# Kernel optimization log

Hardware: AMD Instinct MI355X
Metric: run time of the kernel (lower is better)

The kernel has to match this reference:

```python
import jax, jax.numpy as jnp
import numpy as np

BLOCK = 32      # config.BLOCK_SIZE
PSF_WN = 64     # config.PSF_WINDOW_N (upsampled block size == PSF kernel size)
DX = 1e-06      # config.PIX_SIZE


def images_to_blocks(imgs, B):
    # Faithful to torch reshape/permute chain: block order is (nBW outer, nBH inner)
    N, H, W = imgs.shape
    nBH, nBW = H // B, W // B
    x = imgs.reshape(N, nBH, B, nBW, B)
    x = jnp.transpose(x, (0, 2, 4, 3, 1))        # [N,B,B,nBW,nBH]
    x = x.reshape(N, B, B, nBW * nBH)
    return jnp.transpose(x, (0, 3, 1, 2))        # [N,P,B,B]


def upsample_nearest(blocks, U):
    # torch F.interpolate(mode='nearest'): src index = floor(dst * B / U)
    N, P, B, _ = blocks.shape
    idx = (jnp.arange(U) * B) // U
    return blocks[:, :, idx[:, None], idx[None, :]]  # [N,P,U,U]


def depthwise_full_conv(x, w):
    # per-region cross-correlation with padding K-1 ("full"), groups=P
    N, P, K, _ = x.shape
    return jax.lax.conv_general_dilated(
        x, w[:, None, :, :], window_strides=(1, 1),
        padding=[(K - 1, K - 1), (K - 1, K - 1)],
        dimension_numbers=('NCHW', 'OIHW', 'NCHW'),
        feature_group_count=P)                   # [N,P,2K-1,2K-1]


def splat_blocks_to_sensor(block_out, x_centers, y_centers, X_N, Y_N, dx):
    # Vectorized scatter-add replacing the per-region python loop; out-of-bounds dropped
    N, P, Hk, Wk = block_out.shape
    hk = Hk // 2
    cx, cy = X_N // 2, Y_N // 2
    ic = cx + jnp.round(x_centers / dx).astype(jnp.int32)   # [P]
    jc = cy + jnp.round(y_centers / dx).astype(jnp.int32)
    I = ic[:, None] - hk + jnp.arange(Hk)                   # [P,Hk]
    J = jc[:, None] - hk + jnp.arange(Wk)                   # [P,Wk]
    lin = I[:, :, None] * Y_N + J[:, None, :]               # [P,Hk,Wk]
    ok = ((I >= 0) & (I < X_N))[:, :, None] & ((J >= 0) & (J < Y_N))[:, None, :]
    lin = jnp.where(ok, lin, -1).reshape(-1)
    sensor = jnp.zeros((N, X_N * Y_N), block_out.dtype)
    sensor = sensor.at[:, lin].add(block_out.reshape(N, -1), mode='drop')
    return sensor.reshape(N, X_N, Y_N)


def setup_inputs() -> dict:
    key = jax.random.key(0)
    k1, k2 = jax.random.split(key)
    N, H, W = 8, 512, 512
    P = (H // BLOCK) * (W // BLOCK)   # 256
    X_N = Y_N = 1024
    imgs = jax.random.uniform(k1, (N, H, W), jnp.float32)
    psf_stack = jax.random.uniform(k2, (P, PSF_WN, PSF_WN), jnp.float32)
    psf_stack = psf_stack / jnp.sum(psf_stack, axis=(1, 2), keepdims=True)
    # 16x16 grid of physical region centers, 48-pixel pitch (integer pixels so round() is exact)
    grid = jnp.arange(P)
    rows = (grid % 16).astype(jnp.float32)
    cols = (grid // 16).astype(jnp.float32)
    x_centers = (rows - 7.0) * 48.0 * DX
    y_centers = (cols - 7.0) * 48.0 * DX
    Xg, Yg = jnp.meshgrid(jnp.arange(X_N, dtype=jnp.float32) * DX,
                          jnp.arange(Y_N, dtype=jnp.float32) * DX, indexing='ij')
    return {"imgs": imgs, "psf_stack": psf_stack, "X": Xg, "Y": Yg,
            "x_centers": x_centers, "y_centers": y_centers}


def reference(imgs, psf_stack, X, Y, x_centers, y_centers):
    blocks = images_to_blocks(imgs, BLOCK)               # [N,P,32,32]
    blocks_up = upsample_nearest(blocks, PSF_WN)         # [N,P,64,64]
    block_out = depthwise_full_conv(blocks_up, psf_stack)  # [N,P,127,127]
    X_N, Y_N = X.shape
    return splat_blocks_to_sensor(block_out, x_centers, y_centers, X_N, Y_N, DX)
```

## Files before the change

### kernel.cpp

```cpp
#include <hip/hip_runtime.h>

typedef _Float16 h8 __attribute__((ext_vector_type(8)));
typedef float    f4 __attribute__((ext_vector_type(4)));
typedef unsigned int u4 __attribute__((ext_vector_type(4)));

#define IMG_N 8
#define IMG_H 512
#define IMG_W 512
#define P_CNT 256
#define PSFN  64
#define SENS  1024

#define TILE_HALVES 16256
#define TILES_BYTES ((size_t)IMG_N * P_CNT * TILE_HALVES * 2)

#define KW     90
#define KFRAG_PER_P (4 * 33 * KW)

#define BT_COLS   97
#define BT_HALVES (BT_COLS * 40)

__global__ __launch_bounds__(256) void svconv_prep(
    const float* __restrict__ psf, u4* __restrict__ kfrag)
{
    __shared__ float ps[PSFN * PSFN];
    __shared__ float Kc[4 * 33 * 33];
    const int p = blockIdx.x, tid = threadIdx.x;

    const float4* pp = (const float4*)(psf + (size_t)p * PSFN * PSFN);
    float4* pd = (float4*)ps;
    for (int i = tid; i < PSFN * PSFN / 4; i += 256) pd[i] = pp[i];
    __syncthreads();

    for (int idx = tid; idx < 4 * 33 * 33; idx += 256) {
        const int g = idx % 33, e = (idx / 33) % 33, cls = idx / 1089;
        const int pi = cls >> 1, pj = cls & 1;
        const int E = pi ? 32 : 33;
        float sv = 0.f;
        if (e < E) {
            const int a = 2 * e - 1 + pi, b = 2 * g - 1 + pj;
            #pragma unroll
            for (int du = 0; du < 2; ++du) {
                const int x = a + du;
                if ((unsigned)x < 64u) {
                    #pragma unroll
                    for (int dv = 0; dv < 2; ++dv) {
                        const int y = b + dv;
                        if ((unsigned)y < 64u) sv += ps[x * 64 + y];
                    }
                }
            }
        }
        Kc[idx] = sv;
    }
    __syncthreads();

    u4* kout = kfrag + (size_t)p * KFRAG_PER_P;
    for (int idx = tid; idx < KFRAG_PER_P; idx += 256) {
        const int w = idx % KW;
        const int g = (idx / KW) % 33;
        const int cls = idx / (KW * 33);
        h8 hv;
        #pragma unroll
        for (int j = 0; j < 8; ++j) {
            const int e = w + j - 32;
            const float v = ((unsigned)e < 33u) ? Kc[cls * 1089 + e * 33 + g] : 0.f;
            hv[j] = (_Float16)v;
        }
        kout[idx] = __builtin_bit_cast(u4, hv);
    }
}

__global__ __launch_bounds__(256, 4) void svconv_main(
    const float* __restrict__ imgs, const u4* __restrict__ kfrag,
    _Float16* __restrict__ tiles)
{
    __shared__ __align__(16) _Float16 BT[BT_HALVES];

    const int bid = blockIdx.x;
    const int n = bid >> 8, p = bid & 255;
    const int bh = p & 15, bw = p >> 4;
    const int tid = threadIdx.x;
    const int wv = tid >> 6, lane = tid & 63;
    const int m = lane & 15, q = lane >> 4;

    for (int i = tid; i < BT_HALVES; i += 256) BT[i] = (_Float16)0.f;
    __syncthreads();
    {
        const int r0 = tid >> 5, c = tid & 31;
        const float* src = imgs + ((size_t)n * IMG_H + bh * 32) * IMG_W + bw * 32;
        for (int r = r0; r < 32; r += 8)
            BT[(c + 32) * 40 + r] = (_Float16)src[r * IMG_W + c];
    }
    __syncthreads();

    const int cls = wv, pi = cls >> 1, pj = cls & 1;
    const int U0 = pi ? 31 : 32;
    const char* btc = (const char*)BT + pj * 80;

    int boff[4];
    #pragma unroll
    for (int vt = 0; vt < 4; ++vt) boff[vt] = (16 * vt + m) * 80 + q * 16;

    const char* ka[4];
    {
        const char* base = (const char*)(kfrag + (size_t)p * KFRAG_PER_P
                                         + cls * 33 * KW);
        #pragma unroll
        for (int ut = 0; ut < 4; ++ut) {
            const int t0 = 8 * q - m + (U0 - 16 * ut) + 32;
            ka[ut] = base + t0 * 16;
        }
    }

    f4 acc[4][4];
    #pragma unroll
    for (int ut = 0; ut < 4; ++ut)
        #pragma unroll
        for (int vt = 0; vt < 4; ++vt) acc[ut][vt] = (f4){0.f, 0.f, 0.f, 0.f};

    #pragma unroll 3
    for (int g = 0; g < 33; ++g) {
        h8 A[4];
        #pragma unroll
        for (int ut = 0; ut < 4; ++ut)
            A[ut] = __builtin_bit_cast(h8, *(const u4*)(ka[ut] + g * (KW * 16)));
        h8 B[4];
        #pragma unroll
        for (int vt = 0; vt < 4; ++vt)
            B[vt] = *(const h8*)(btc + boff[vt] + g * 80);
        #pragma unroll
        for (int ut = 0; ut < 4; ++ut)
            #pragma unroll
            for (int vt = 0; vt < 4; ++vt)
                acc[ut][vt] = __builtin_amdgcn_mfma_f32_16x16x32_f16(
                    A[ut], B[vt], acc[ut][vt], 0, 0, 0);
    }

    _Float16* tile = tiles + (size_t)(n * P_CNT + p) * TILE_HALVES;
    const int plane = pi ? (8192 + pj * 4032) : (pj * 4096);
    #pragma unroll
    for (int ut = 0; ut < 4; ++ut) {
        #pragma unroll
        for (int reg = 0; reg < 4; ++reg) {
            const int u = 16 * ut + 4 * q + reg;
            if (pi == 0 || u < 63) {
                _Float16* rp = tile + plane + u * 64 + m;
                #pragma unroll
                for (int vt = 0; vt < 4; ++vt)
                    rp[16 * vt] = (_Float16)acc[ut][vt][reg];
            }
        }
    }
}

__global__ __launch_bounds__(256) void svconv_gather(
    const _Float16* __restrict__ ws, float* __restrict__ out)
{
    const int b = blockIdx.x;
    const int n = b >> 10, x = b & 1023;
    int bhlo = (x + 288) / 48 - 10; if (bhlo < 0) bhlo = 0;
    int bhhi = (x < 113) ? -1 : ((x - 113) / 48);
    if (bhhi > 15) bhhi = 15;
    const _Float16* wsn = ws + (size_t)n * P_CNT * TILE_HALVES;
    float* outrow = out + ((size_t)n << 20) + (size_t)x * SENS;

    for (int yb = 0; yb < 4; ++yb) {
        const int y = yb * 256 + threadIdx.x;
        int bwlo = (y + 288) / 48 - 10; if (bwlo < 0) bwlo = 0;
        int bwhi = (y < 113) ? -1 : ((y - 113) / 48);
        if (bwhi > 15) bwhi = 15;
        float s = 0.0f;
        for (int bhh = bhlo; bhh <= bhhi; ++bhh) {
            const int ti = x - 113 - 48 * bhh;
            const int pi = ti & 1, uu = ti >> 1;
            for (int bww = bwlo; bww <= bwhi; ++bww) {
                const int tj = y - 113 - 48 * bww;
                const int pj = tj & 1, vv = tj >> 1;
                const int base = pi ? (8192 + pj * 4032) : (pj * 4096);
                s += (float)wsn[(size_t)(bww * 16 + bhh) * TILE_HALVES
                                + base + uu * 64 + vv];
            }
        }
        outrow[y] = s;
    }
}

extern "C" void kernel_launch(void* const* d_in, const int* in_sizes, int n_in,
                              void* d_out, int out_size, void* d_ws, size_t ws_size,
                              hipStream_t stream) {
    const float* imgs = (const float*)d_in[0];
    const float* psf  = (const float*)d_in[1];
    float* out = (float*)d_out;
    _Float16* tiles = (_Float16*)d_ws;
    u4* kfrag = (u4*)((char*)d_ws + TILES_BYTES);

    svconv_prep<<<dim3(P_CNT), dim3(256), 0, stream>>>(psf, kfrag);
    svconv_main<<<dim3(IMG_N * P_CNT), dim3(256), 0, stream>>>(imgs, kfrag, tiles);
    svconv_gather<<<dim3(IMG_N * SENS), dim3(256), 0, stream>>>(tiles, out);
}
```

Before: 228.3 us.

## Stage gather tile rows in LDS, double-buffer kernel fragments, split prep

The gather kernel now loads the up to 3x16 tile rows each output row needs into shared memory with 16-byte vector loads, then sums overlapping tiles from LDS. Out-of-range tiles are redirected to a zero slot instead of looping with variable bounds. This replaces scattered 2-byte global reads. The main MFMA loop is fully unrolled with double-buffered register prefetch of the A fragments to hide global load latency. The prep kernel is split across 4x more blocks for parallelism. Risks are higher register pressure in main and redundant Kc recomputation in prep.

```diff
diff --git a/kernel.cpp b/kernel.cpp
--- a/kernel.cpp
+++ b/kernel.cpp
@@ -15,6 +15,7 @@
 #define TILES_BYTES ((size_t)IMG_N * P_CNT * TILE_HALVES * 2)
 
 #define KW     90
+#define KWB    (KW * 16)
 #define KFRAG_PER_P (4 * 33 * KW)
 
 #define BT_COLS   97
@@ -25,7 +26,7 @@
 {
     __shared__ float ps[PSFN * PSFN];
     __shared__ float Kc[4 * 33 * 33];
-    const int p = blockIdx.x, tid = threadIdx.x;
+    const int p = blockIdx.x >> 2, q4 = blockIdx.x & 3, tid = threadIdx.x;
 
     const float4* pp = (const float4*)(psf + (size_t)p * PSFN * PSFN);
     float4* pd = (float4*)ps;
@@ -56,7 +57,8 @@
     __syncthreads();
 
     u4* kout = kfrag + (size_t)p * KFRAG_PER_P;
-    for (int idx = tid; idx < KFRAG_PER_P; idx += 256) {
+    for (int i2 = tid; i2 < KFRAG_PER_P / 4; i2 += 256) {
+        const int idx = q4 * (KFRAG_PER_P / 4) + i2;
         const int w = idx % KW;
         const int g = (idx / KW) % 33;
         const int cls = idx / (KW * 33);
@@ -119,23 +121,44 @@
         #pragma unroll
         for (int vt = 0; vt < 4; ++vt) acc[ut][vt] = (f4){0.f, 0.f, 0.f, 0.f};
 
-    #pragma unroll 3
-    for (int g = 0; g < 33; ++g) {
-        h8 A[4];
-        #pragma unroll
-        for (int ut = 0; ut < 4; ++ut)
-            A[ut] = __builtin_bit_cast(h8, *(const u4*)(ka[ut] + g * (KW * 16)));
-        h8 B[4];
-        #pragma unroll
-        for (int vt = 0; vt < 4; ++vt)
-            B[vt] = *(const h8*)(btc + boff[vt] + g * 80);
-        #pragma unroll
-        for (int ut = 0; ut < 4; ++ut)
-            #pragma unroll
-            for (int vt = 0; vt < 4; ++vt)
-                acc[ut][vt] = __builtin_amdgcn_mfma_f32_16x16x32_f16(
-                    A[ut], B[vt], acc[ut][vt], 0, 0, 0);
-    }
+    u4 A0[4], A1[4];
+    #pragma unroll
+    for (int ut = 0; ut < 4; ++ut) A0[ut] = *(const u4*)(ka[ut]);
+    #pragma unroll
+    for (int ut = 0; ut < 4; ++ut) A1[ut] = *(const u4*)(ka[ut] + KWB);
+
+    #define DO_G(Abuf, G)                                                     \
+        {                                                                     \
+            h8 B[4];                                                          \
+            _Pragma("unroll")                                                 \
+            for (int vt = 0; vt < 4; ++vt)                                    \
+                B[vt] = *(const h8*)(btc + boff[vt] + (G) * 80);              \
+            _Pragma("unroll")                                                 \
+            for (int ut = 0; ut < 4; ++ut)                                    \
+                _Pragma("unroll")                                             \
+                for (int vt = 0; vt < 4; ++vt)                                \
+                    acc[ut][vt] = __builtin_amdgcn_mfma_f32_16x16x32_f16(     \
+                        __builtin_bit_cast(h8, Abuf[ut]), B[vt],              \
+                        acc[ut][vt], 0, 0, 0);                                \
+        }
+
+    #pragma unroll
+    for (int gg = 0; gg < 16; ++gg) {
+        DO_G(A0, 2 * gg);
+        if (2 * gg + 2 < 33) {
+            #pragma unroll
+            for (int ut = 0; ut < 4; ++ut)
+                A0[ut] = *(const u4*)(ka[ut] + (2 * gg + 2) * KWB);
+        }
+        DO_G(A1, 2 * gg + 1);
+        if (2 * gg + 3 < 33) {
+            #pragma unroll
+            for (int ut = 0; ut < 4; ++ut)
+                A1[ut] = *(const u4*)(ka[ut] + (2 * gg + 3) * KWB);
+        }
+    }
+    DO_G(A0, 32);
+    #undef DO_G
 
     _Float16* tile = tiles + (size_t)(n * P_CNT + p) * TILE_HALVES;
     const int plane = pi ? (8192 + pj * 4032) : (pj * 4096);
@@ -154,32 +177,57 @@
     }
 }
 
+#define LROWS 96
+#define ZOFF  (LROWS * 64)
+
 __global__ __launch_bounds__(256) void svconv_gather(
-    const _Float16* __restrict__ ws, float* __restrict__ out)
+    const _Float16* __restrict__ tiles, float* __restrict__ out)
 {
+    __shared__ __align__(16) _Float16 Ls[ZOFF + 64];
+
     const int b = blockIdx.x;
     const int n = b >> 10, x = b & 1023;
+    const int tid = threadIdx.x;
+
     int bhlo = (x + 288) / 48 - 10; if (bhlo < 0) bhlo = 0;
-    int bhhi = (x < 113) ? -1 : ((x - 113) / 48);
-    if (bhhi > 15) bhhi = 15;
-    const _Float16* wsn = ws + (size_t)n * P_CNT * TILE_HALVES;
+    const int bhhi = (x < 113) ? -1 : (((x - 113) / 48) > 15 ? 15 : (x - 113) / 48);
+    const _Float16* tn = tiles + (size_t)n * P_CNT * TILE_HALVES;
+
+    if (tid < 8) ((u4*)&Ls[ZOFF])[tid] = (u4){0u, 0u, 0u, 0u};
+    for (int c = tid; c < LROWS * 8; c += 256) {
+        const int rid = c >> 3, w = c & 7;
+        const int k3 = rid >> 5, rem = rid & 31, bww = rem >> 1, pjj = rem & 1;
+        const int bhh = bhlo + k3;
+        u4 val = (u4){0u, 0u, 0u, 0u};
+        if (bhh <= bhhi) {
+            const int ti = x - 113 - 48 * bhh;
+            const int pii = ti & 1, uu = ti >> 1;
+            const int base = (pii ? (8192 + pjj * 4032) : (pjj * 4096)) + uu * 64;
+            val = *(const u4*)(tn + (size_t)(bww * 16 + bhh) * TILE_HALVES
+                               + base + w * 8);
+        }
+        *(u4*)&Ls[rid * 64 + w * 8] = val;
+    }
+    __syncthreads();
+
     float* outrow = out + ((size_t)n << 20) + (size_t)x * SENS;
-
+    #pragma unroll
     for (int yb = 0; yb < 4; ++yb) {
-        const int y = yb * 256 + threadIdx.x;
+        const int y = yb * 256 + tid;
         int bwlo = (y + 288) / 48 - 10; if (bwlo < 0) bwlo = 0;
-        int bwhi = (y < 113) ? -1 : ((y - 113) / 48);
-        if (bwhi > 15) bwhi = 15;
+        const int bwhi = (y < 113) ? -1 : (((y - 113) / 48) > 15 ? 15 : (y - 113) / 48);
+        const int t0 = y - 113 - 48 * bwlo;
         float s = 0.0f;
-        for (int bhh = bhlo; bhh <= bhhi; ++bhh) {
-            const int ti = x - 113 - 48 * bhh;
-            const int pi = ti & 1, uu = ti >> 1;
-            for (int bww = bwlo; bww <= bwhi; ++bww) {
-                const int tj = y - 113 - 48 * bww;
-                const int pj = tj & 1, vv = tj >> 1;
-                const int base = pi ? (8192 + pj * 4032) : (pj * 4096);
-                s += (float)wsn[(size_t)(bww * 16 + bhh) * TILE_HALVES
-                                + base + uu * 64 + vv];
+        #pragma unroll
+        for (int k3 = 0; k3 < 3; ++k3) {
+            #pragma unroll
+            for (int kw = 0; kw < 3; ++kw) {
+                const int bww = bwlo + kw;
+                const int tj = t0 - 48 * kw;
+                const int pjj = tj & 1, vv = tj >> 1;
+                int idx = k3 * 2048 + (bww * 2 + pjj) * 64 + vv;
+                idx = (bww <= bwhi) ? idx : ZOFF;
+                s += (float)Ls[idx];
             }
         }
         outrow[y] = s;
@@ -195,7 +243,7 @@
     _Float16* tiles = (_Float16*)d_ws;
     u4* kfrag = (u4*)((char*)d_ws + TILES_BYTES);
 
-    svconv_prep<<<dim3(P_CNT), dim3(256), 0, stream>>>(psf, kfrag);
+    svconv_prep<<<dim3(P_CNT * 4), dim3(256), 0, stream>>>(psf, kfrag);
     svconv_main<<<dim3(IMG_N * P_CNT), dim3(256), 0, stream>>>(imgs, kfrag, tiles);
     svconv_gather<<<dim3(IMG_N * SENS), dim3(256), 0, stream>>>(tiles, out);
 }
```

Result: slower. 379.6 us (+66.3%).
